# Performance work log

Measured on AMD Instinct MI355X. Metric: run time of the kernel, lower is better.

Reference implementation:

```python
import jax, jax.numpy as jnp
import numpy as np
from jax import lax

H = 256       # GRU/LSTM hidden size
E = 32        # word embedding dim
VOCAB = 128000
MAX_EP = 1000
P_LEN, C_LEN, N_LEN = 512, 256, 512
FH = FW = 6
IMG_FLAT = 64 * FH * FW  # 2304


def _gru(xs, wih, whh, bih, bhh):
    # torch nn.GRU semantics, gate order [r; z; n]; xs: (T, E) -> (T, H)
    gi = xs @ wih.T + bih  # (T, 3H), precompute input projections
    def step(h, g):
        gh = h @ whh.T + bhh
        ir, iz, inn = jnp.split(g, 3)
        hr, hz, hn = jnp.split(gh, 3)
        r = jax.nn.sigmoid(ir + hr)
        z = jax.nn.sigmoid(iz + hz)
        n = jnp.tanh(inn + r * hn)
        h2 = (1.0 - z) * n + z * h
        return h2, h2
    _, hs = lax.scan(step, jnp.zeros((H,), xs.dtype), gi)
    return hs


def _conv(x, w, b, s):
    y = lax.conv_general_dilated(x, w, (s, s), 'VALID',
                                 dimension_numbers=('NCHW', 'OIHW', 'NCHW'))
    return y + b[None, :, None, None]


def setup_inputs() -> dict:
    key = jax.random.key(0)
    ks = iter(jax.random.split(key, 64))
    def w(shape, s=0.02):
        return jax.random.normal(next(ks), shape, jnp.float32) * s
    inp = {}
    inp['x'] = jax.random.normal(next(ks), (1, 3, 124, 124), jnp.float32)
    inp['hx'] = jax.random.normal(next(ks), (1, H), jnp.float32) * 0.1
    inp['cx'] = jax.random.normal(next(ks), (1, H), jnp.float32) * 0.1
    inp['prev_inst'] = jax.random.randint(next(ks), (1, P_LEN), 0, VOCAB)
    inp['curr_inst'] = jax.random.randint(next(ks), (1, C_LEN), 0, VOCAB)
    inp['next_inst'] = jax.random.randint(next(ks), (1, N_LEN), 0, VOCAB)
    inp['tx'] = jax.random.randint(next(ks), (1,), 0, MAX_EP + 1)
    # parameters
    inp['emb'] = w((VOCAB, E), 0.05)
    # GRU order: [f_prev, f_curr, f_next, b_prev, b_curr, b_next]
    inp['gru_wih'] = w((6, 3 * H, E))
    inp['gru_whh'] = w((6, 3 * H, H))
    inp['gru_bih'] = w((6, 3 * H), 0.01)
    inp['gru_bhh'] = w((6, 3 * H), 0.01)
    inp['conv1_w'] = w((128, 3, 8, 8));   inp['conv1_b'] = w((128,), 0.01)
    inp['conv2_w'] = w((64, 128, 4, 4));  inp['conv2_b'] = w((64,), 0.01)
    inp['conv3_w'] = w((64, 64, 4, 4));   inp['conv3_b'] = w((64,), 0.01)
    inp['img_w'] = w((256, IMG_FLAT));    inp['img_b'] = w((256,), 0.01)
    inp['akp_w'] = w((256, 768));         inp['akp_b'] = w((256,), 0.01)
    inp['akn_w'] = w((256, 768));         inp['akn_b'] = w((256,), 0.01)
    inp['bil_p_w'] = w((1, 256, 512));    inp['bil_p_b'] = w((1,), 0.01)
    inp['bil_n_w'] = w((1, 256, 512));    inp['bil_n_b'] = w((1,), 0.01)
    inp['pred_w'] = w((64, 512));         inp['pred_b'] = w((64,), 0.01)
    inp['nred_w'] = w((64, 512));         inp['nred_b'] = w((64,), 0.01)
    inp['gate_w'] = w((64, 512 + 128));   inp['gate_b'] = w((64,), 0.01)
    inp['lin_w'] = w((256, IMG_FLAT));    inp['lin_b'] = w((256,), 0.01)
    inp['lstm_wih'] = w((4 * H, 256));    inp['lstm_whh'] = w((4 * H, H))
    inp['lstm_bih'] = jnp.zeros((4 * H,), jnp.float32)
    inp['lstm_bhh'] = jnp.zeros((4 * H,), jnp.float32)
    inp['time_emb'] = w((MAX_EP + 1, E), 0.05)
    inp['crit_w'] = w((1, 256 + E));      inp['crit_b'] = jnp.zeros((1,), jnp.float32)
    inp['act_w'] = w((4, 256 + E), 0.01); inp['act_b'] = jnp.zeros((4,), jnp.float32)
    return inp


def reference(x, hx, cx, prev_inst, curr_inst, next_inst, tx, emb,
              gru_wih, gru_whh, gru_bih, gru_bhh,
              conv1_w, conv1_b, conv2_w, conv2_b, conv3_w, conv3_b,
              img_w, img_b, akp_w, akp_b, akn_w, akn_b,
              bil_p_w, bil_p_b, bil_n_w, bil_n_b,
              pred_w, pred_b, nred_w, nred_b, gate_w, gate_b,
              lin_w, lin_b, lstm_wih, lstm_whh, lstm_bih, lstm_bhh,
              time_emb, crit_w, crit_b, act_w, act_b):
    # CNN tower
    x1 = jax.nn.relu(_conv(x, conv1_w, conv1_b, 4))
    x2 = jax.nn.relu(_conv(x1, conv2_w, conv2_b, 2))
    x_img = jax.nn.relu(_conv(x2, conv3_w, conv3_b, 2))  # (1,64,6,6)

    ep = emb[prev_inst[0]]  # (P, E)
    ec = emb[curr_inst[0]]  # (C, E)
    en = emb[next_inst[0]]  # (N, E)
    P, C, N = ep.shape[0], ec.shape[0], en.shape[0]

    def run(j, e):
        return _gru(e, gru_wih[j], gru_whh[j], gru_bih[j], gru_bhh[j])
    hf = jnp.concatenate([run(0, ep), run(1, ec), run(2, en)], 0)  # (T, H)
    hb = jnp.concatenate([run(3, ep), run(4, ec), run(5, en)], 0)
    rb = hb[::-1]  # source reverses only the collected hidden list

    curr_rep = jnp.concatenate([hf[P + C - 1], rb[P]])[None]        # (1, 512)
    prev_rep = jnp.concatenate([hf[:P], rb[:P]], 1)                  # (P, 512)
    next_rep = jnp.concatenate([hf[P + C:], rb[P + C:]], 1)          # (N, 512)

    image_emb = x_img.reshape(1, -1) @ img_w.T + img_b               # (1, 256)
    ak_in = jnp.concatenate([curr_rep, image_emb], 1)                # (1, 768)

    def attend(ak_w, ak_b, bw, bb, rep):
        k = (ak_in @ ak_w.T + ak_b)[0]           # (256,) shared key
        s = (k @ bw[0]) @ rep.T + bb[0]          # (L,) bilinear scores
        wgt = jax.nn.softmax(s)
        return wgt @ rep                          # (512,)

    prev_sum = attend(akp_w, akp_b, bil_p_w, bil_p_b, prev_rep)
    next_sum = attend(akn_w, akn_b, bil_n_w, bil_n_b, next_rep)
    pg = prev_sum @ pred_w.T + pred_b            # (64,)
    ng = next_sum @ nred_w.T + nred_b            # (64,)

    gate_in = jnp.concatenate([curr_rep[0], pg, ng])[None]  # (1, 640)
    gate = jax.nn.sigmoid(gate_in @ gate_w.T + gate_b)      # (1, 64)

    xg = (x_img * gate[:, :, None, None]).reshape(1, -1)
    feat = jax.nn.relu(xg @ lin_w.T + lin_b)                # (1, 256)

    # torch LSTMCell, gate order [i; f; g; o]
    g = feat @ lstm_wih.T + lstm_bih + hx @ lstm_whh.T + lstm_bhh
    i, f, gg, o = jnp.split(g, 4, axis=1)
    cx2 = jax.nn.sigmoid(f) * cx + jax.nn.sigmoid(i) * jnp.tanh(gg)
    hx2 = jax.nn.sigmoid(o) * jnp.tanh(cx2)

    te = time_emb[tx].reshape(1, E)
    z = jnp.concatenate([hx2, te], 1)                       # (1, 288)
    return (z @ crit_w.T + crit_b, z @ act_w.T + act_b, hx2, cx2)
```

## Files before the change

kernel.cpp:

```cpp
#include <hip/hip_runtime.h>
#include <hip/hip_bf16.h>

typedef unsigned int u32;
typedef _Float16 f16x8 __attribute__((ext_vector_type(8)));
typedef float f32x4 __attribute__((ext_vector_type(4)));

__device__ __forceinline__ float sigf(float x){ return 1.0f/(1.0f + __expf(-x)); }

#define GI_OFF   0
#define GI_SZ    (2560*768)
#define HF_OFF   (GI_OFF + GI_SZ)
#define HF_SZ    (1280*256)
#define HB_OFF   (HF_OFF + HF_SZ)
#define X1_OFF   (HB_OFF + HF_SZ)
#define X1_SZ    (128*30*30)
#define X2_OFF   (X1_OFF + X1_SZ)
#define X2_SZ    (64*14*14)
#define XIMG_OFF (X2_OFF + X2_SZ)
#define XIMG_SZ  (64*6*6)
#define AKIN_OFF (XIMG_OFF + XIMG_SZ)
#define PSUM_OFF (AKIN_OFF + 768)
#define NSUM_OFF (PSUM_OFF + 512)

__global__ __launch_bounds__(256) void gi_kernel(
    const float* __restrict__ emb, const float* __restrict__ wih_all,
    const float* __restrict__ bih_all,
    const int* __restrict__ prev, const int* __restrict__ curr, const int* __restrict__ nxt,
    float* __restrict__ gi_all)
{
  const int offs[7] = {0,512,768,1280,1792,2048,2560};
  int row0 = blockIdx.x * 16;
  int j = 0;
  while (row0 >= offs[j+1]) ++j;
  int t0 = row0 - offs[j];
  int sel = j % 3;
  const int* inst = (sel==0)? prev : (sel==1)? curr : nxt;

  __shared__ __align__(16) float e[16][32];
  int u = threadIdx.x;
  for (int idx=u; idx<512; idx+=256){
    int r = idx >> 5, k = idx & 31;
    e[r][k] = emb[(size_t)inst[t0+r]*32 + k];
  }
  __syncthreads();

  const float* wih = wih_all + (size_t)j*768*32;
  const float* bih = bih_all + (size_t)j*768;
  for (int g3=0; g3<3; ++g3){
    int o = g3*256 + u;
    float bb = bih[o];
    float acc[16];
#pragma unroll
    for (int r=0;r<16;++r) acc[r]=bb;
    const float* wr = wih + (size_t)o*32;
#pragma unroll
    for (int k=0;k<32;++k){
      float w = wr[k];
#pragma unroll
      for (int r=0;r<16;++r) acc[r] += w * e[r][k];
    }
    for (int r=0;r<16;++r) gi_all[(size_t)(row0+r)*768 + o] = acc[r];
  }
}

__global__ __launch_bounds__(512,2) void gru_scan_kernel(
    const float* __restrict__ whh_all, const float* __restrict__ bhh_all,
    const float* __restrict__ gi_all, float* __restrict__ hf, float* __restrict__ hb)
{
  const int lens[6] = {512,256,512,512,256,512};
  const int offs[6] = {0,512,768,1280,1792,2048};
  int j = blockIdx.x;
  int u = threadIdx.x;
  int len = lens[j];
  const float* gi = gi_all + (size_t)offs[j]*768;
  float* outp = ((j<3)? hf : hb) + (size_t)offs[j%3]*256;

  int w    = u >> 6;
  int l    = u & 63;
  int arow = l & 15;
  int kgrp = l >> 4;

  f16x8 af[6][8];
  {
    const float* Wj = whh_all + (size_t)j*768*256;
#pragma unroll
    for (int i=0;i<6;++i){
      const float* wrow = Wj + (size_t)(16*(w*6+i) + arow)*256;
#pragma unroll
      for (int kt=0;kt<8;++kt){
        const float4* p = (const float4*)(wrow + 32*kt + 8*kgrp);
        float4 c0 = p[0], c1 = p[1];
        f16x8 v;
        v[0]=(_Float16)c0.x; v[1]=(_Float16)c0.y; v[2]=(_Float16)c0.z; v[3]=(_Float16)c0.w;
        v[4]=(_Float16)c1.x; v[5]=(_Float16)c1.y; v[6]=(_Float16)c1.z; v[7]=(_Float16)c1.w;
        af[i][kt] = v;
      }
    }
  }

  float bh0=0.f, bh1=0.f, bh2=0.f, hprev=0.f;
  if (u < 256){
    bh0 = bhh_all[j*768 + u];
    bh1 = bhh_all[j*768 + 256 + u];
    bh2 = bhh_all[j*768 + 512 + u];
  }

  __shared__ __align__(16) _Float16 h16[256];
  __shared__ __align__(16) float gacc[768];
  if (u < 256) h16[u] = (_Float16)0.0f;
  __syncthreads();

  for (int t=0; t<len; ++t){
    float gr=0.f, gz=0.f, gn=0.f;
    if (u < 256){
      const float* git = gi + (size_t)t*768;
      gr = git[u]; gz = git[256+u]; gn = git[512+u];
    }

    f32x4 acc[6];
#pragma unroll
    for (int i=0;i<6;++i){ f32x4 zz = {0.f,0.f,0.f,0.f}; acc[i] = zz; }
#pragma unroll
    for (int kt=0; kt<8; ++kt){
      f16x8 bfr = *(const f16x8*)(h16 + 32*kt + 8*kgrp);
#pragma unroll
      for (int i=0;i<6;++i)
        acc[i] = __builtin_amdgcn_mfma_f32_16x16x32_f16(af[i][kt], bfr, acc[i], 0, 0, 0);
    }
    if (arow == 0){
#pragma unroll
      for (int i=0;i<6;++i){
        float4 v; v.x=acc[i][0]; v.y=acc[i][1]; v.z=acc[i][2]; v.w=acc[i][3];
        *(float4*)&gacc[16*(w*6+i) + 4*kgrp] = v;
      }
    }
    __syncthreads();

    if (u < 256){
      float r  = sigf(gr + bh0 + gacc[u]);
      float z  = sigf(gz + bh1 + gacc[256+u]);
      float n  = tanhf(gn + bh2 + r*gacc[512+u]);
      float h2 = (1.0f - z)*n + z*hprev;
      outp[(size_t)t*256 + u] = h2;
      h16[u] = (_Float16)h2;
      hprev = h2;
    }
    __syncthreads();
  }
}

__global__ __launch_bounds__(256) void conv1_kernel(
    const float* __restrict__ x, const float* __restrict__ w, const float* __restrict__ b,
    float* __restrict__ y)
{
  int idx = blockIdx.x*256 + threadIdx.x;
  if (idx >= 128*30*30) return;
  int c = idx/900, rem = idx%900, i = rem/30, jx = rem%30;
  float acc = b[c];
  const float* wc = w + (size_t)c*3*8*8;
  for (int ic=0; ic<3; ++ic)
    for (int ky=0; ky<8; ++ky){
      const float* xrow = x + ((size_t)ic*124 + (i*4+ky))*124 + jx*4;
      const float* wrow = wc + (ic*8+ky)*8;
#pragma unroll
      for (int kx=0; kx<8; ++kx) acc += xrow[kx] * wrow[kx];
    }
  y[idx] = fmaxf(acc, 0.0f);
}

__global__ __launch_bounds__(256) void conv2_kernel(
    const float* __restrict__ x1, const float* __restrict__ w, const float* __restrict__ b,
    float* __restrict__ y)
{
  int idx = blockIdx.x*256 + threadIdx.x;
  if (idx >= 64*14*14) return;
  int c = idx/196, rem = idx%196, i = rem/14, jx = rem%14;
  float acc = b[c];
  for (int ic=0; ic<128; ++ic){
    const float* xc = x1 + (size_t)ic*900;
    const float* wc = w + ((size_t)c*128 + ic)*16;
#pragma unroll
    for (int ky=0; ky<4; ++ky)
#pragma unroll
      for (int kx=0; kx<4; ++kx)
        acc += xc[(i*2+ky)*30 + (jx*2+kx)] * wc[ky*4+kx];
  }
  y[idx] = fmaxf(acc, 0.0f);
}

__global__ __launch_bounds__(256) void conv3_kernel(
    const float* __restrict__ x2, const float* __restrict__ w, const float* __restrict__ b,
    float* __restrict__ y)
{
  int idx = blockIdx.x*256 + threadIdx.x;
  if (idx >= 64*6*6) return;
  int c = idx/36, rem = idx%36, i = rem/6, jx = rem%6;
  float acc = b[c];
  for (int ic=0; ic<64; ++ic){
    const float* xc = x2 + (size_t)ic*196;
    const float* wc = w + ((size_t)c*64 + ic)*16;
#pragma unroll
    for (int ky=0; ky<4; ++ky)
#pragma unroll
      for (int kx=0; kx<4; ++kx)
        acc += xc[(i*2+ky)*14 + (jx*2+kx)] * wc[ky*4+kx];
  }
  y[idx] = fmaxf(acc, 0.0f);
}

__global__ __launch_bounds__(256) void imgemb_kernel(
    const float* __restrict__ x_img, const float* __restrict__ img_w, const float* __restrict__ img_b,
    const float* __restrict__ hf, const float* __restrict__ hb, float* __restrict__ ak_in)
{
  __shared__ __align__(16) float xs[2304];
  int u = threadIdx.x;
  for (int i=u; i<2304; i+=256) xs[i] = x_img[i];
  __syncthreads();
  float a0=0.f,a1=0.f,a2=0.f,a3=0.f;
  const float4* wr = (const float4*)(img_w + (size_t)u*2304);
  const float4* xv = (const float4*)xs;
  for (int k=0; k<576; ++k){
    float4 w = wr[k], xx = xv[k];
    a0 += w.x*xx.x; a1 += w.y*xx.y; a2 += w.z*xx.z; a3 += w.w*xx.w;
  }
  ak_in[512+u] = img_b[u] + ((a0+a1)+(a2+a3));
  ak_in[u]     = hf[(size_t)767*256+u];
  ak_in[256+u] = hb[(size_t)767*256+u];
}

__global__ __launch_bounds__(512) void attend_kernel(
    const float* __restrict__ ak_in_g,
    const float* __restrict__ akp_w, const float* __restrict__ akp_b,
    const float* __restrict__ akn_w, const float* __restrict__ akn_b,
    const float* __restrict__ bil_p_w, const float* __restrict__ bil_p_b,
    const float* __restrict__ bil_n_w, const float* __restrict__ bil_n_b,
    const float* __restrict__ hf, const float* __restrict__ hb,
    float* __restrict__ prev_sum, float* __restrict__ next_sum)
{
  int blk = blockIdx.x;
  const float* akw = blk? akn_w : akp_w;
  const float* akb = blk? akn_b : akp_b;
  const float* bw  = blk? bil_n_w : bil_p_w;
  float bb         = blk? bil_n_b[0] : bil_p_b[0];
  float* outp      = blk? next_sum : prev_sum;

  int u = threadIdx.x;
  __shared__ __align__(16) float ak[768];
  __shared__ __align__(16) float kk[256];
  __shared__ __align__(16) float q[512];
  __shared__ float s[512], red[512];

  for (int i=u; i<768; i+=512) ak[i] = ak_in_g[i];
  __syncthreads();

  if (u < 256){
    float a0=0.f,a1=0.f,a2=0.f,a3=0.f;
    const float4* wr = (const float4*)(akw + (size_t)u*768);
    const float4* av = (const float4*)ak;
    for (int m=0; m<192; ++m){
      float4 w = wr[m], aa = av[m];
      a0 += w.x*aa.x; a1 += w.y*aa.y; a2 += w.z*aa.z; a3 += w.w*aa.w;
    }
    kk[u] = akb[u] + ((a0+a1)+(a2+a3));
  }
  __syncthreads();

  {
    float acc = 0.0f;
    for (int m=0; m<256; ++m) acc += kk[m]*bw[(size_t)m*512 + u];
    q[u] = acc;
  }
  __syncthreads();

  {
    int i = u;
    const float4* repf = (const float4*)(hf + (size_t)(blk? (768+i) : i)*256);
    const float4* repb = (const float4*)(hb + (size_t)(blk? (511-i) : (1279-i))*256);
    const float4* qf = (const float4*)q;
    float a0=0.f,a1=0.f;
    for (int v=0; v<64; ++v){
      float4 qq = qf[v],  rr = repf[v];
      a0 += qq.x*rr.x + qq.y*rr.y + qq.z*rr.z + qq.w*rr.w;
      float4 q2 = qf[64+v], r2 = repb[v];
      a1 += q2.x*r2.x + q2.y*r2.y + q2.z*r2.z + q2.w*r2.w;
    }
    s[u] = bb + a0 + a1;
  }
  __syncthreads();

  red[u] = s[u]; __syncthreads();
  for (int st=256; st>0; st>>=1){ if (u<st) red[u]=fmaxf(red[u],red[u+st]); __syncthreads(); }
  float mx = red[0]; __syncthreads();
  float ex = __expf(s[u]-mx);
  red[u] = ex; __syncthreads();
  for (int st=256; st>0; st>>=1){ if (u<st) red[u]+=red[u+st]; __syncthreads(); }
  float inv = 1.0f/red[0]; __syncthreads();
  s[u] = ex*inv;
  __syncthreads();

  float o = 0.0f;
  if (u < 256){
    for (int r=0; r<512; ++r){
      const float* rf = hf + (size_t)(blk? (768+r) : r)*256;
      o += s[r]*rf[u];
    }
    outp[u] = o;
  } else {
    int v = u-256;
    for (int r=0; r<512; ++r){
      const float* rb = hb + (size_t)(blk? (511-r) : (1279-r))*256;
      o += s[r]*rb[v];
    }
    outp[u] = o;
  }
}

__global__ __launch_bounds__(1024) void head_kernel(
    const float* __restrict__ prev_sum_g, const float* __restrict__ next_sum_g,
    const float* __restrict__ ak_in_g, const float* __restrict__ x_img,
    const float* __restrict__ pred_w, const float* __restrict__ pred_b,
    const float* __restrict__ nred_w, const float* __restrict__ nred_b,
    const float* __restrict__ gate_w, const float* __restrict__ gate_b,
    const float* __restrict__ lin_w,  const float* __restrict__ lin_b,
    const float* __restrict__ lstm_wih, const float* __restrict__ lstm_whh,
    const float* __restrict__ lstm_bih, const float* __restrict__ lstm_bhh,
    const float* __restrict__ hx, const float* __restrict__ cx,
    const int* __restrict__ tx, const float* __restrict__ time_emb,
    const float* __restrict__ crit_w, const float* __restrict__ crit_b,
    const float* __restrict__ act_w,  const float* __restrict__ act_b,
    float* __restrict__ out)
{
  int u = threadIdx.x;
  __shared__ __align__(16) float ps[512];
  __shared__ __align__(16) float ns[512];
  __shared__ __align__(16) float cr[512];
  __shared__ float pg[64], ng[64], gate[64];
  __shared__ __align__(16) float xg[2304];
  __shared__ __align__(16) float feat[256];
  __shared__ __align__(16) float hxs[256];
  __shared__ float g[1024], cxs[256], z[288];

  if (u < 512){ ps[u]=prev_sum_g[u]; ns[u]=next_sum_g[u]; cr[u]=ak_in_g[u]; }
  if (u >= 512 && u < 768){ int t=u-512; hxs[t]=hx[t]; cxs[t]=cx[t]; }
  for (int i=u; i<2304; i+=1024) xg[i] = x_img[i];
  __syncthreads();

  if (u < 64){
    float a = pred_b[u];
    const float* wr = pred_w + (size_t)u*512;
    for (int k=0;k<512;++k) a += ps[k]*wr[k];
    pg[u] = a;
  } else if (u < 128){
    int t = u-64;
    float a = nred_b[t];
    const float* wr = nred_w + (size_t)t*512;
    for (int k=0;k<512;++k) a += ns[k]*wr[k];
    ng[t] = a;
  }
  __syncthreads();

  if (u < 64){
    float a = gate_b[u];
    const float* wr = gate_w + (size_t)u*640;
    for (int k=0;k<512;++k) a += cr[k]*wr[k];
    for (int k=0;k<64;++k)  a += pg[k]*wr[512+k];
    for (int k=0;k<64;++k)  a += ng[k]*wr[576+k];
    gate[u] = sigf(a);
  }
  __syncthreads();

  for (int i=u; i<2304; i+=1024) xg[i] *= gate[i/36];
  __syncthreads();

  if (u < 256){
    float a0=0.f,a1=0.f,a2=0.f,a3=0.f;
    const float4* wr = (const float4*)(lin_w + (size_t)u*2304);
    const float4* xv = (const float4*)xg;
    for (int k=0;k<576;++k){
      float4 w = wr[k], xx = xv[k];
      a0 += w.x*xx.x; a1 += w.y*xx.y; a2 += w.z*xx.z; a3 += w.w*xx.w;
    }
    feat[u] = fmaxf(lin_b[u] + ((a0+a1)+(a2+a3)), 0.0f);
  }
  __syncthreads();

  {
    float a0=0.f,a1=0.f;
    const float4* w1 = (const float4*)(lstm_wih + (size_t)u*256);
    const float4* w2 = (const float4*)(lstm_whh + (size_t)u*256);
    const float4* fv = (const float4*)feat;
    const float4* hv = (const float4*)hxs;
    for (int k=0;k<64;++k){
      float4 wa = w1[k], fa = fv[k];
      a0 += wa.x*fa.x + wa.y*fa.y + wa.z*fa.z + wa.w*fa.w;
      float4 wb = w2[k], ha = hv[k];
      a1 += wb.x*ha.x + wb.y*ha.y + wb.z*ha.z + wb.w*ha.w;
    }
    g[u] = lstm_bih[u] + lstm_bhh[u] + a0 + a1;
  }
  __syncthreads();

  if (u < 256){
    float ii=g[u], ff=g[256+u], gg=g[512+u], oo=g[768+u];
    float c2 = sigf(ff)*cxs[u] + sigf(ii)*tanhf(gg);
    float h2 = sigf(oo)*tanhf(c2);
    z[u] = h2;
    out[5+u]   = h2;
    out[261+u] = c2;
  }
  if (u >= 256 && u < 288){
    int e2 = u-256;
    z[u] = time_emb[(size_t)tx[0]*32 + e2];
  }
  __syncthreads();

  if (u == 0){
    float a = crit_b[0];
    for (int k=0;k<288;++k) a += z[k]*crit_w[k];
    out[0] = a;
  } else if (u < 5){
    int r = u-1;
    float a = act_b[r];
    for (int k=0;k<288;++k) a += z[k]*act_w[(size_t)r*288+k];
    out[1+r] = a;
  }
}

extern "C" void kernel_launch(void* const* d_in, const int* in_sizes, int n_in,
                              void* d_out, int out_size, void* d_ws, size_t ws_size,
                              hipStream_t stream)
{
  const float* x        = (const float*)d_in[0];
  const float* hx       = (const float*)d_in[1];
  const float* cx       = (const float*)d_in[2];
  const int*  prev      = (const int*)d_in[3];
  const int*  curr      = (const int*)d_in[4];
  const int*  nxt       = (const int*)d_in[5];
  const int*  tx        = (const int*)d_in[6];
  const float* emb      = (const float*)d_in[7];
  const float* gru_wih  = (const float*)d_in[8];
  const float* gru_whh  = (const float*)d_in[9];
  const float* gru_bih  = (const float*)d_in[10];
  const float* gru_bhh  = (const float*)d_in[11];
  const float* conv1_w  = (const float*)d_in[12];
  const float* conv1_b  = (const float*)d_in[13];
  const float* conv2_w  = (const float*)d_in[14];
  const float* conv2_b  = (const float*)d_in[15];
  const float* conv3_w  = (const float*)d_in[16];
  const float* conv3_b  = (const float*)d_in[17];
  const float* img_w    = (const float*)d_in[18];
  const float* img_b    = (const float*)d_in[19];
  const float* akp_w    = (const float*)d_in[20];
  const float* akp_b    = (const float*)d_in[21];
  const float* akn_w    = (const float*)d_in[22];
  const float* akn_b    = (const float*)d_in[23];
  const float* bil_p_w  = (const float*)d_in[24];
  const float* bil_p_b  = (const float*)d_in[25];
  const float* bil_n_w  = (const float*)d_in[26];
  const float* bil_n_b  = (const float*)d_in[27];
  const float* pred_w   = (const float*)d_in[28];
  const float* pred_b   = (const float*)d_in[29];
  const float* nred_w   = (const float*)d_in[30];
  const float* nred_b   = (const float*)d_in[31];
  const float* gate_w   = (const float*)d_in[32];
  const float* gate_b   = (const float*)d_in[33];
  const float* lin_w    = (const float*)d_in[34];
  const float* lin_b    = (const float*)d_in[35];
  const float* lstm_wih = (const float*)d_in[36];
  const float* lstm_whh = (const float*)d_in[37];
  const float* lstm_bih = (const float*)d_in[38];
  const float* lstm_bhh = (const float*)d_in[39];
  const float* time_emb = (const float*)d_in[40];
  const float* crit_w   = (const float*)d_in[41];
  const float* crit_b   = (const float*)d_in[42];
  const float* act_w    = (const float*)d_in[43];
  const float* act_b    = (const float*)d_in[44];

  float* ws = (float*)d_ws;
  float* gi    = ws + GI_OFF;
  float* hf    = ws + HF_OFF;
  float* hb    = ws + HB_OFF;
  float* x1    = ws + X1_OFF;
  float* x2    = ws + X2_OFF;
  float* ximg  = ws + XIMG_OFF;
  float* akin  = ws + AKIN_OFF;
  float* psum  = ws + PSUM_OFF;
  float* nsum  = ws + NSUM_OFF;

  float* out = (float*)d_out;

  gi_kernel      <<<160, 256, 0, stream>>>(emb, gru_wih, gru_bih, prev, curr, nxt, gi);
  gru_scan_kernel<<<6,   512, 0, stream>>>(gru_whh, gru_bhh, gi, hf, hb);
  conv1_kernel   <<<450, 256, 0, stream>>>(x, conv1_w, conv1_b, x1);
  conv2_kernel   <<<49,  256, 0, stream>>>(x1, conv2_w, conv2_b, x2);
  conv3_kernel   <<<9,   256, 0, stream>>>(x2, conv3_w, conv3_b, ximg);
  imgemb_kernel  <<<1,   256, 0, stream>>>(ximg, img_w, img_b, hf, hb, akin);
  attend_kernel  <<<2,   512, 0, stream>>>(akin, akp_w, akp_b, akn_w, akn_b,
                                           bil_p_w, bil_p_b, bil_n_w, bil_n_b,
                                           hf, hb, psum, nsum);
  head_kernel    <<<1,  1024, 0, stream>>>(psum, nsum, akin, ximg,
                                           pred_w, pred_b, nred_w, nred_b,
                                           gate_w, gate_b, lin_w, lin_b,
                                           lstm_wih, lstm_whh, lstm_bih, lstm_bhh,
                                           hx, cx, tx, time_emb,
                                           crit_w, crit_b, act_w, act_b, out);
}
```

Measured before the change: 1.134 ms.

## Shrink GRU scan block, parallelize head GEMVs across blocks, fast tanh

The GRU recurrence now runs with 256 threads per block, each wave holding twice as many fp16 weight fragments in registers. All threads do the gate math, and output stores are deferred one step off the critical path. A fast exp-based tanh replaces tanhf. The image-embedding GEMV and the single-block head kernel are split into multi-block, warp-reduced kernels (head_a, lin, lstm, final) so the large GEMVs use more CUs. The cost is higher register pressure in the scan and a few extra kernel launches.

```diff
diff --git a/kernel.cpp b/kernel.cpp
--- a/kernel.cpp
+++ b/kernel.cpp
@@ -6,6 +6,11 @@
 typedef float f32x4 __attribute__((ext_vector_type(4)));
 
 __device__ __forceinline__ float sigf(float x){ return 1.0f/(1.0f + __expf(-x)); }
+__device__ __forceinline__ float tanhfast(float x){
+  float xc = fminf(fmaxf(x, -15.0f), 15.0f);
+  float e = __expf(2.0f*xc);
+  return (e - 1.0f)/(e + 1.0f);
+}
 
 #define GI_OFF   0
 #define GI_SZ    (2560*768)
@@ -21,6 +26,9 @@
 #define AKIN_OFF (XIMG_OFF + XIMG_SZ)
 #define PSUM_OFF (AKIN_OFF + 768)
 #define NSUM_OFF (PSUM_OFF + 512)
+#define GATE_OFF (NSUM_OFF + 512)
+#define FEAT_OFF (GATE_OFF + 64)
+#define G_OFF    (FEAT_OFF + 256)
 
 __global__ __launch_bounds__(256) void gi_kernel(
     const float* __restrict__ emb, const float* __restrict__ wih_all,
@@ -63,7 +71,7 @@
   }
 }
 
-__global__ __launch_bounds__(512,2) void gru_scan_kernel(
+__global__ __launch_bounds__(256,1) void gru_scan_kernel(
     const float* __restrict__ whh_all, const float* __restrict__ bhh_all,
     const float* __restrict__ gi_all, float* __restrict__ hf, float* __restrict__ hb)
 {
@@ -80,12 +88,12 @@
   int arow = l & 15;
   int kgrp = l >> 4;
 
-  f16x8 af[6][8];
+  f16x8 af[12][8];
   {
     const float* Wj = whh_all + (size_t)j*768*256;
 #pragma unroll
-    for (int i=0;i<6;++i){
-      const float* wrow = Wj + (size_t)(16*(w*6+i) + arow)*256;
+    for (int i=0;i<12;++i){
+      const float* wrow = Wj + (size_t)(16*(w*12+i) + arow)*256;
 #pragma unroll
       for (int kt=0;kt<8;++kt){
         const float4* p = (const float4*)(wrow + 32*kt + 8*kgrp);
@@ -98,55 +106,52 @@
     }
   }
 
-  float bh0=0.f, bh1=0.f, bh2=0.f, hprev=0.f;
-  if (u < 256){
-    bh0 = bhh_all[j*768 + u];
-    bh1 = bhh_all[j*768 + 256 + u];
-    bh2 = bhh_all[j*768 + 512 + u];
-  }
+  float bh0 = bhh_all[j*768 + u];
+  float bh1 = bhh_all[j*768 + 256 + u];
+  float bh2 = bhh_all[j*768 + 512 + u];
+  float hprev = 0.0f;
 
   __shared__ __align__(16) _Float16 h16[256];
   __shared__ __align__(16) float gacc[768];
-  if (u < 256) h16[u] = (_Float16)0.0f;
+  h16[u] = (_Float16)0.0f;
   __syncthreads();
 
   for (int t=0; t<len; ++t){
-    float gr=0.f, gz=0.f, gn=0.f;
-    if (u < 256){
-      const float* git = gi + (size_t)t*768;
-      gr = git[u]; gz = git[256+u]; gn = git[512+u];
-    }
-
-    f32x4 acc[6];
-#pragma unroll
-    for (int i=0;i<6;++i){ f32x4 zz = {0.f,0.f,0.f,0.f}; acc[i] = zz; }
-#pragma unroll
-    for (int kt=0; kt<8; ++kt){
-      f16x8 bfr = *(const f16x8*)(h16 + 32*kt + 8*kgrp);
-#pragma unroll
-      for (int i=0;i<6;++i)
-        acc[i] = __builtin_amdgcn_mfma_f32_16x16x32_f16(af[i][kt], bfr, acc[i], 0, 0, 0);
-    }
-    if (arow == 0){
-#pragma unroll
-      for (int i=0;i<6;++i){
-        float4 v; v.x=acc[i][0]; v.y=acc[i][1]; v.z=acc[i][2]; v.w=acc[i][3];
-        *(float4*)&gacc[16*(w*6+i) + 4*kgrp] = v;
+    if (t > 0) outp[(size_t)(t-1)*256 + u] = hprev;
+    const float* git = gi + (size_t)t*768;
+    float gr = git[u], gz = git[256+u], gn = git[512+u];
+
+#pragma unroll
+    for (int g=0; g<3; ++g){
+      f32x4 acc[4];
+#pragma unroll
+      for (int i=0;i<4;++i){ f32x4 zz = {0.f,0.f,0.f,0.f}; acc[i] = zz; }
+#pragma unroll
+      for (int kt=0; kt<8; ++kt){
+        f16x8 bfr = *(const f16x8*)(h16 + 32*kt + 8*kgrp);
+#pragma unroll
+        for (int i=0;i<4;++i)
+          acc[i] = __builtin_amdgcn_mfma_f32_16x16x32_f16(af[g*4+i][kt], bfr, acc[i], 0, 0, 0);
       }
+      if (arow == 0){
+#pragma unroll
+        for (int i=0;i<4;++i){
+          float4 v; v.x=acc[i][0]; v.y=acc[i][1]; v.z=acc[i][2]; v.w=acc[i][3];
+          *(float4*)&gacc[16*(w*12 + g*4 + i) + 4*kgrp] = v;
+        }
+      }
     }
     __syncthreads();
 
-    if (u < 256){
-      float r  = sigf(gr + bh0 + gacc[u]);
-      float z  = sigf(gz + bh1 + gacc[256+u]);
-      float n  = tanhf(gn + bh2 + r*gacc[512+u]);
-      float h2 = (1.0f - z)*n + z*hprev;
-      outp[(size_t)t*256 + u] = h2;
-      h16[u] = (_Float16)h2;
-      hprev = h2;
-    }
+    float r  = sigf(gr + bh0 + gacc[u]);
+    float z  = sigf(gz + bh1 + gacc[256+u]);
+    float n  = tanhfast(gn + bh2 + r*gacc[512+u]);
+    float h2 = (1.0f - z)*n + z*hprev;
+    h16[u] = (_Float16)h2;
+    hprev = h2;
     __syncthreads();
   }
+  outp[(size_t)(len-1)*256 + u] = hprev;
 }
 
 __global__ __launch_bounds__(256) void conv1_kernel(
@@ -212,20 +217,19 @@
     const float* __restrict__ x_img, const float* __restrict__ img_w, const float* __restrict__ img_b,
     const float* __restrict__ hf, const float* __restrict__ hb, float* __restrict__ ak_in)
 {
-  __shared__ __align__(16) float xs[2304];
-  int u = threadIdx.x;
-  for (int i=u; i<2304; i+=256) xs[i] = x_img[i];
-  __syncthreads();
-  float a0=0.f,a1=0.f,a2=0.f,a3=0.f;
-  const float4* wr = (const float4*)(img_w + (size_t)u*2304);
-  const float4* xv = (const float4*)xs;
-  for (int k=0; k<576; ++k){
-    float4 w = wr[k], xx = xv[k];
-    a0 += w.x*xx.x; a1 += w.y*xx.y; a2 += w.z*xx.z; a3 += w.w*xx.w;
-  }
-  ak_in[512+u] = img_b[u] + ((a0+a1)+(a2+a3));
-  ak_in[u]     = hf[(size_t)767*256+u];
-  ak_in[256+u] = hb[(size_t)767*256+u];
+  int u = threadIdx.x;
+  int r = blockIdx.x*8 + (u>>5);
+  int lane = u & 31;
+  const float* wr = img_w + (size_t)r*2304;
+  float acc = 0.0f;
+  for (int k=lane; k<2304; k+=32) acc += wr[k]*x_img[k];
+#pragma unroll
+  for (int m=16; m; m>>=1) acc += __shfl_xor(acc, m, 64);
+  if (lane == 0) ak_in[512+r] = img_b[r] + acc;
+  if (blockIdx.x == 0){
+    ak_in[u]     = hf[(size_t)767*256+u];
+    ak_in[256+u] = hb[(size_t)767*256+u];
+  }
 }
 
 __global__ __launch_bounds__(512) void attend_kernel(
@@ -315,34 +319,18 @@
   }
 }
 
-__global__ __launch_bounds__(1024) void head_kernel(
-    const float* __restrict__ prev_sum_g, const float* __restrict__ next_sum_g,
-    const float* __restrict__ ak_in_g, const float* __restrict__ x_img,
+__global__ __launch_bounds__(256) void head_a_kernel(
+    const float* __restrict__ psum, const float* __restrict__ nsum,
+    const float* __restrict__ akin,
     const float* __restrict__ pred_w, const float* __restrict__ pred_b,
     const float* __restrict__ nred_w, const float* __restrict__ nred_b,
     const float* __restrict__ gate_w, const float* __restrict__ gate_b,
-    const float* __restrict__ lin_w,  const float* __restrict__ lin_b,
-    const float* __restrict__ lstm_wih, const float* __restrict__ lstm_whh,
-    const float* __restrict__ lstm_bih, const float* __restrict__ lstm_bhh,
-    const float* __restrict__ hx, const float* __restrict__ cx,
-    const int* __restrict__ tx, const float* __restrict__ time_emb,
-    const float* __restrict__ crit_w, const float* __restrict__ crit_b,
-    const float* __restrict__ act_w,  const float* __restrict__ act_b,
-    float* __restrict__ out)
-{
-  int u = threadIdx.x;
-  __shared__ __align__(16) float ps[512];
-  __shared__ __align__(16) float ns[512];
-  __shared__ __align__(16) float cr[512];
-  __shared__ float pg[64], ng[64], gate[64];
-  __shared__ __align__(16) float xg[2304];
-  __shared__ __align__(16) float feat[256];
-  __shared__ __align__(16) float hxs[256];
-  __shared__ float g[1024], cxs[256], z[288];
-
-  if (u < 512){ ps[u]=prev_sum_g[u]; ns[u]=next_sum_g[u]; cr[u]=ak_in_g[u]; }
-  if (u >= 512 && u < 768){ int t=u-512; hxs[t]=hx[t]; cxs[t]=cx[t]; }
-  for (int i=u; i<2304; i+=1024) xg[i] = x_img[i];
+    float* __restrict__ gate_out)
+{
+  int u = threadIdx.x;
+  __shared__ __align__(16) float ps[512], ns[512], cr[512];
+  __shared__ float pg[64], ng[64];
+  for (int i=u; i<512; i+=256){ ps[i]=psum[i]; ns[i]=nsum[i]; cr[i]=akin[i]; }
   __syncthreads();
 
   if (u < 64){
@@ -365,64 +353,84 @@
     for (int k=0;k<512;++k) a += cr[k]*wr[k];
     for (int k=0;k<64;++k)  a += pg[k]*wr[512+k];
     for (int k=0;k<64;++k)  a += ng[k]*wr[576+k];
-    gate[u] = sigf(a);
-  }
-  __syncthreads();
-
-  for (int i=u; i<2304; i+=1024) xg[i] *= gate[i/36];
-  __syncthreads();
-
-  if (u < 256){
-    float a0=0.f,a1=0.f,a2=0.f,a3=0.f;
-    const float4* wr = (const float4*)(lin_w + (size_t)u*2304);
-    const float4* xv = (const float4*)xg;
-    for (int k=0;k<576;++k){
-      float4 w = wr[k], xx = xv[k];
-      a0 += w.x*xx.x; a1 += w.y*xx.y; a2 += w.z*xx.z; a3 += w.w*xx.w;
-    }
-    feat[u] = fmaxf(lin_b[u] + ((a0+a1)+(a2+a3)), 0.0f);
-  }
-  __syncthreads();
-
-  {
-    float a0=0.f,a1=0.f;
-    const float4* w1 = (const float4*)(lstm_wih + (size_t)u*256);
-    const float4* w2 = (const float4*)(lstm_whh + (size_t)u*256);
-    const float4* fv = (const float4*)feat;
-    const float4* hv = (const float4*)hxs;
-    for (int k=0;k<64;++k){
-      float4 wa = w1[k], fa = fv[k];
-      a0 += wa.x*fa.x + wa.y*fa.y + wa.z*fa.z + wa.w*fa.w;
-      float4 wb = w2[k], ha = hv[k];
-      a1 += wb.x*ha.x + wb.y*ha.y + wb.z*ha.z + wb.w*ha.w;
-    }
-    g[u] = lstm_bih[u] + lstm_bhh[u] + a0 + a1;
-  }
-  __syncthreads();
-
+    gate_out[u] = sigf(a);
+  }
+}
+
+__global__ __launch_bounds__(256) void lin_kernel(
+    const float* __restrict__ x_img, const float* __restrict__ gate,
+    const float* __restrict__ lin_w, const float* __restrict__ lin_b,
+    float* __restrict__ feat)
+{
+  int u = threadIdx.x;
+  __shared__ __align__(16) float xg[2304];
+  for (int i=u; i<2304; i+=256) xg[i] = x_img[i]*gate[i/36];
+  __syncthreads();
+
+  int r = blockIdx.x*8 + (u>>5);
+  int lane = u & 31;
+  const float* wr = lin_w + (size_t)r*2304;
+  float acc = 0.0f;
+  for (int k=lane; k<2304; k+=32) acc += wr[k]*xg[k];
+#pragma unroll
+  for (int m=16; m; m>>=1) acc += __shfl_xor(acc, m, 64);
+  if (lane == 0) feat[r] = fmaxf(lin_b[r] + acc, 0.0f);
+}
+
+__global__ __launch_bounds__(256) void lstm_kernel(
+    const float* __restrict__ feat, const float* __restrict__ hx,
+    const float* __restrict__ wih, const float* __restrict__ whh,
+    const float* __restrict__ bih, const float* __restrict__ bhh,
+    float* __restrict__ g)
+{
+  int u = threadIdx.x;
+  __shared__ __align__(16) float fs[256], hs[256];
+  fs[u] = feat[u]; hs[u] = hx[u];
+  __syncthreads();
+  int row = blockIdx.x*256 + u;
+  float a0=0.f, a1=0.f;
+  const float4* w1 = (const float4*)(wih + (size_t)row*256);
+  const float4* w2 = (const float4*)(whh + (size_t)row*256);
+  const float4* fv = (const float4*)fs;
+  const float4* hv = (const float4*)hs;
+  for (int k=0;k<64;++k){
+    float4 wa = w1[k], fa = fv[k];
+    a0 += wa.x*fa.x + wa.y*fa.y + wa.z*fa.z + wa.w*fa.w;
+    float4 wb = w2[k], ha = hv[k];
+    a1 += wb.x*ha.x + wb.y*ha.y + wb.z*ha.z + wb.w*ha.w;
+  }
+  g[row] = bih[row] + bhh[row] + a0 + a1;
+}
+
+__global__ __launch_bounds__(320) void final_kernel(
+    const float* __restrict__ g, const float* __restrict__ cx,
+    const int* __restrict__ tx, const float* __restrict__ time_emb,
+    const float* __restrict__ crit_w, const float* __restrict__ crit_b,
+    const float* __restrict__ act_w,  const float* __restrict__ act_b,
+    float* __restrict__ out)
+{
+  int u = threadIdx.x;
+  __shared__ float z[320];
   if (u < 256){
     float ii=g[u], ff=g[256+u], gg=g[512+u], oo=g[768+u];
-    float c2 = sigf(ff)*cxs[u] + sigf(ii)*tanhf(gg);
-    float h2 = sigf(oo)*tanhf(c2);
-    z[u] = h2;
+    float c2 = sigf(ff)*cx[u] + sigf(ii)*tanhfast(gg);
+    float h2 = sigf(oo)*tanhfast(c2);
     out[5+u]   = h2;
     out[261+u] = c2;
-  }
-  if (u >= 256 && u < 288){
-    int e2 = u-256;
-    z[u] = time_emb[(size_t)tx[0]*32 + e2];
-  }
-  __syncthreads();
-
-  if (u == 0){
-    float a = crit_b[0];
-    for (int k=0;k<288;++k) a += z[k]*crit_w[k];
-    out[0] = a;
-  } else if (u < 5){
-    int r = u-1;
-    float a = act_b[r];
-    for (int k=0;k<288;++k) a += z[k]*act_w[(size_t)r*288+k];
-    out[1+r] = a;
+    z[u] = h2;
+  } else if (u < 288){
+    z[u] = time_emb[(size_t)tx[0]*32 + (u-256)];
+  }
+  __syncthreads();
+  int row = u >> 6, lane = u & 63;
+  const float* wv = (row==0)? crit_w : (act_w + (size_t)(row-1)*288);
+  float acc = 0.0f;
+  for (int k=lane; k<288; k+=64) acc += wv[k]*z[k];
+#pragma unroll
+  for (int m=32; m; m>>=1) acc += __shfl_xor(acc, m, 64);
+  if (lane == 0){
+    float b = (row==0)? crit_b[0] : act_b[row-1];
+    out[row] = acc + b;
   }
 }
 
@@ -486,22 +494,27 @@
   float* akin  = ws + AKIN_OFF;
   float* psum  = ws + PSUM_OFF;
   float* nsum  = ws + NSUM_OFF;
+  float* gatev = ws + GATE_OFF;
+  float* featv = ws + FEAT_OFF;
+  float* gvec  = ws + G_OFF;
 
   float* out = (float*)d_out;
 
   gi_kernel      <<<160, 256, 0, stream>>>(emb, gru_wih, gru_bih, prev, curr, nxt, gi);
-  gru_scan_kernel<<<6,   512, 0, stream>>>(gru_whh, gru_bhh, gi, hf, hb);
+  gru_scan_kernel<<<6,   256, 0, stream>>>(gru_whh, gru_bhh, gi, hf, hb);
   conv1_kernel   <<<450, 256, 0, stream>>>(x, conv1_w, conv1_b, x1);
   conv2_kernel   <<<49,  256, 0, stream>>>(x1, conv2_w, conv2_b, x2);
   conv3_kernel   <<<9,   256, 0, stream>>>(x2, conv3_w, conv3_b, ximg);
-  imgemb_kernel  <<<1,   256, 0, stream>>>(ximg, img_w, img_b, hf, hb, akin);
+  imgemb_kernel  <<<32,  256, 0, stream>>>(ximg, img_w, img_b, hf, hb, akin);
   attend_kernel  <<<2,   512, 0, stream>>>(akin, akp_w, akp_b, akn_w, akn_b,
                                            bil_p_w, bil_p_b, bil_n_w, bil_n_b,
                                            hf, hb, psum, nsum);
-  head_kernel    <<<1,  1024, 0, stream>>>(psum, nsum, akin, ximg,
+  head_a_kernel  <<<1,   256, 0, stream>>>(psum, nsum, akin,
                                            pred_w, pred_b, nred_w, nred_b,
-                                           gate_w, gate_b, lin_w, lin_b,
-                                           lstm_wih, lstm_whh, lstm_bih, lstm_bhh,
-                                           hx, cx, tx, time_emb,
+                                           gate_w, gate_b, gatev);
+  lin_kernel     <<<32,  256, 0, stream>>>(ximg, gatev, lin_w, lin_b, featv);
+  lstm_kernel    <<<4,   256, 0, stream>>>(featv, hx, lstm_wih, lstm_whh,
+                                           lstm_bih, lstm_bhh, gvec);
+  final_kernel   <<<1,   320, 0, stream>>>(gvec, cx, tx, time_emb,
                                            crit_w, crit_b, act_w, act_b, out);
 }
```

Result: faster. 1.098 ms (-3.2%).
